# Kernel optimization log

Measured on AMD Instinct MI355X. Metric: run time of the kernel, lower is better.

## Reference

```python
import jax, jax.numpy as jnp
import numpy as np
from jax import lax

B, S, E, H = 8, 1024, 1024, 16
HEAD_DIM = E // H
THRESHOLD = 0.5
NEG_FILL = -1e9


def setup_inputs() -> dict:
    key = jax.random.key(0)
    k0, k1, k2 = jax.random.split(key, 3)
    x = jax.random.normal(k0, (B, S, E), jnp.float32)
    in_proj_w = jax.random.normal(k1, (3 * E, E), jnp.float32) * 0.02
    in_proj_b = jnp.zeros((3 * E,), jnp.float32)
    out_proj_w = jax.random.normal(k2, (E, E), jnp.float32) * 0.02
    out_proj_b = jnp.zeros((E,), jnp.float32)
    return {"x": x, "in_proj_w": in_proj_w, "in_proj_b": in_proj_b,
            "out_proj_w": out_proj_w, "out_proj_b": out_proj_b}


def _mha(x, in_proj_w, in_proj_b, out_proj_w, out_proj_b):
    # PyTorch nn.MultiheadAttention with q=k=v=x, batch_first=True
    qkv = x @ in_proj_w.T + in_proj_b                     # [B,S,3E]
    q, k, v = jnp.split(qkv, 3, axis=-1)                  # each [B,S,E]
    def split_heads(t):
        return t.reshape(B, S, H, HEAD_DIM).transpose(0, 2, 1, 3)  # [B,H,S,d]
    q, k, v = split_heads(q), split_heads(k), split_heads(v)
    scale = 1.0 / np.sqrt(HEAD_DIM).astype(np.float32)
    scores = jnp.einsum('bhqd,bhkd->bhqk', q, k) * scale  # [B,H,S,S]
    w = jax.nn.softmax(scores, axis=-1)
    o = jnp.einsum('bhqk,bhkd->bhqd', w, v)               # [B,H,S,d]
    o = o.transpose(0, 2, 1, 3).reshape(B, S, E)
    attn_output = o @ out_proj_w.T + out_proj_b           # [B,S,E]
    attn_weights = w.mean(axis=1)                         # head-averaged [B,S,S]
    return attn_output, attn_weights


def _cluster(attn_weights):
    # Sequential greedy clustering: scan rows i in order; if row i is not yet
    # visited, its high-attention columns (> THRESHOLD) form cluster i and are
    # marked visited. cluster_id[b, j] = row index of the first cluster that
    # claimed token j, or -1 if never claimed.
    visited0 = jnp.zeros((B, S), dtype=bool)
    cid0 = jnp.full((B, S), -1, dtype=jnp.int32)

    def step(carry, i):
        visited, cid = carry
        process = ~jnp.take(visited, i, axis=1)           # [B] row i unvisited?
        high = jnp.take(attn_weights, i, axis=1) > THRESHOLD  # [B,S]
        claimed = process[:, None] & high                 # [B,S]
        newly = claimed & (~visited)
        cid = jnp.where(newly, jnp.int32(i), cid)
        visited = visited | claimed
        return (visited, cid), None

    (visited, cid), _ = lax.scan(step, (visited0, cid0), jnp.arange(S))
    return cid, visited


def reference(x, in_proj_w, in_proj_b, out_proj_w, out_proj_b):
    attn_output, attn_weights = _mha(x, in_proj_w, in_proj_b, out_proj_w, out_proj_b)
    cluster_ids, covered = _cluster(attn_weights)
    # _generate_image_features: x where token belongs to some cluster, -1e9 else
    clustered_outputs = jnp.where(covered[..., None], x, jnp.float32(NEG_FILL))
    return attn_output, attn_weights, clustered_outputs, cluster_ids
```

## Files before the change

kernel.cpp:

```cpp
#include <hip/hip_runtime.h>
#include <hip/hip_bf16.h>

#define B 8
#define S 1024
#define E 1024
#define H 16

typedef unsigned short u16;
typedef unsigned char u8;
typedef unsigned int u32;
typedef unsigned long long u64;

typedef __attribute__((ext_vector_type(8))) short s16x8;
typedef __attribute__((ext_vector_type(4))) float f32x4;
typedef __attribute__((ext_vector_type(16))) float f32x16;

__device__ __forceinline__ float bf2f(u16 u) {
    union { u32 i; float f; } x; x.i = ((u32)u) << 16; return x.f;
}
__device__ __forceinline__ u16 f2bf(float f) {
    union { float f; u32 i; } x; x.f = f;
    u32 r = x.i + 0x7FFFu + ((x.i >> 16) & 1u);
    return (u16)(r >> 16);
}
__device__ __forceinline__ f32x16 zero16() {
    f32x16 z;
#pragma unroll
    for (int i = 0; i < 16; ++i) z[i] = 0.f;
    return z;
}
__device__ __forceinline__ void gload16(const u16* g, u16* l) {
    __builtin_amdgcn_global_load_lds(
        (const __attribute__((address_space(1))) u32*)g,
        (__attribute__((address_space(3))) u32*)l, 16, 0, 0);
}

__global__ __launch_bounds__(256) void cvt_all(
    const float* __restrict__ x, const float* __restrict__ w0,
    const float* __restrict__ w1, u16* __restrict__ xb,
    u16* __restrict__ wb0, u16* __restrict__ wb1) {
    int i = blockIdx.x * 256 + threadIdx.x;
    const float* src;
    u16* dst;
    int off;
    if (i < 2097152) { src = x; dst = xb; off = i; }
    else if (i < 2883584) { src = w0; dst = wb0; off = i - 2097152; }
    else { src = w1; dst = wb1; off = i - 2883584; }
    float4 v = ((const float4*)src)[off];
    union { u16 u[4]; ushort4 s; } p;
    p.u[0] = f2bf(v.x); p.u[1] = f2bf(v.y);
    p.u[2] = f2bf(v.z); p.u[3] = f2bf(v.w);
    ((ushort4*)dst)[off] = p.s;
}

template <int MODE>
__global__ __launch_bounds__(256) void mfma_gemm(
    const u16* __restrict__ A, const u16* __restrict__ W,
    const float* __restrict__ bias, u16* __restrict__ qb, u16* __restrict__ kb,
    u16* __restrict__ vt, float* __restrict__ outf) {
    __shared__ __align__(16) u16 smem[16384];
    u16* As = smem;
    u16* Bs = smem + 8192;
    const int t = threadIdx.x;
    const int lane = t & 63;
    const int w = t >> 6;
    const int lin = (int)(blockIdx.y * gridDim.x + blockIdx.x);
    const int xcd = lin & 7;
    const int idx = lin >> 3;
    int mt, nt;
    if (MODE == 0) { mt = (xcd & 3) * 16 + idx / 12; nt = (xcd >> 2) * 12 + idx % 12; }
    else           { mt = xcd * 8 + idx / 8;         nt = idx % 8; }
    const int m0 = mt * 128;
    const int n0 = nt * 128;
    const int wm = w >> 1, wn = w & 1;
    const int l15 = lane & 15, l4 = lane >> 4;
    const int lr = lane >> 3;
    const int lc = ((lane & 7) ^ lr) * 8;

    f32x4 acc[4][4];
#pragma unroll
    for (int i = 0; i < 4; ++i)
#pragma unroll
        for (int j = 0; j < 4; ++j) acc[i][j] = {0.f, 0.f, 0.f, 0.f};

    for (int k0 = 0; k0 < 1024; k0 += 64) {
        __syncthreads();
#pragma unroll
        for (int jj = 0; jj < 4; ++jj) {
            int j = w * 4 + jj;
            gload16(A + (size_t)(m0 + j * 8 + lr) * 1024 + k0 + lc, As + j * 512);
            gload16(W + (size_t)(n0 + j * 8 + lr) * 1024 + k0 + lc, Bs + j * 512);
        }
        __syncthreads();
#pragma unroll
        for (int ks = 0; ks < 2; ++ks) {
            s16x8 af[4], bf[4];
#pragma unroll
            for (int i = 0; i < 4; ++i) {
                int row = wm * 64 + i * 16 + l15;
                af[i] = *(const s16x8*)((const u8*)As +
                        (((row << 7) + (ks << 6) + (l4 << 4)) ^ ((row & 7) << 4)));
            }
#pragma unroll
            for (int j = 0; j < 4; ++j) {
                int row = wn * 64 + j * 16 + l15;
                bf[j] = *(const s16x8*)((const u8*)Bs +
                        (((row << 7) + (ks << 6) + (l4 << 4)) ^ ((row & 7) << 4)));
            }
#pragma unroll
            for (int i = 0; i < 4; ++i)
#pragma unroll
                for (int j = 0; j < 4; ++j)
                    acc[i][j] = __builtin_amdgcn_mfma_f32_16x16x32_bf16(
                        af[i], bf[j], acc[i][j], 0, 0, 0);
        }
    }

    if (MODE == 0) {
        __syncthreads();
        u16* Cs = smem;
        const int seg = n0 >> 10;
        const int bb = m0 >> 10;
        const int ms = m0 & 1023;
        if (seg < 2) {
            const float sc = (seg == 0) ? 0.18033688011f : 1.0f;
#pragma unroll
            for (int j = 0; j < 4; ++j) {
                int nl = wn * 64 + j * 16 + l15;
                float bn = bias[n0 + nl];
#pragma unroll
                for (int i = 0; i < 4; ++i) {
                    int ml = wm * 64 + i * 16 + l4 * 4;
#pragma unroll
                    for (int rr = 0; rr < 4; ++rr)
                        Cs[(ml + rr) * 128 + nl] = f2bf((acc[i][j][rr] + bn) * sc);
                }
            }
            __syncthreads();
            u16* dst0 = (seg == 0) ? qb : kb;
#pragma unroll
            for (int it = 0; it < 8; ++it) {
                int flat = it * 256 + t;
                int ml = flat >> 4;
                int g = (flat >> 3) & 1;
                int c8 = flat & 7;
                int hh = ((n0 + g * 64) & 1023) >> 6;
                u16* dst = dst0 + (((size_t)(bb * 16 + hh) * 1024 + ms + ml) << 6) + c8 * 8;
                *(uint4*)dst = *(const uint4*)(Cs + ml * 128 + g * 64 + c8 * 8);
            }
        } else {
#pragma unroll
            for (int j = 0; j < 4; ++j) {
                int nl = wn * 64 + j * 16 + l15;
                float bn = bias[n0 + nl];
                int sz = (nl & 7) << 4;
#pragma unroll
                for (int i = 0; i < 4; ++i) {
                    int ml = wm * 64 + i * 16 + l4 * 4;
#pragma unroll
                    for (int rr = 0; rr < 4; ++rr) {
                        int bl = (ml + rr) << 1;
                        *(u16*)((u8*)Cs + (nl << 8) + (bl ^ sz)) =
                            f2bf(acc[i][j][rr] + bn);
                    }
                }
            }
            __syncthreads();
#pragma unroll
            for (int it = 0; it < 8; ++it) {
                int flat = it * 256 + t;
                int nl = flat >> 4;
                int c = flat & 15;
                int n = n0 + nl;
                int hh = (n & 1023) >> 6;
                int d = n & 63;
                u16* dst = vt + ((size_t)(bb * 16 + hh) * 64 + d) * 1024 + ms + c * 8;
                *(uint4*)dst = *(const uint4*)((u8*)Cs + (nl << 8) +
                                               ((c << 4) ^ ((nl & 7) << 4)));
            }
        }
    } else {
        __syncthreads();
        float* Csf = (float*)smem;
#pragma unroll
        for (int r = 0; r < 2; ++r) {
            if (wm == r) {
#pragma unroll
                for (int j = 0; j < 4; ++j) {
                    int nl = wn * 64 + j * 16 + l15;
                    float bn = bias[n0 + nl];
#pragma unroll
                    for (int i = 0; i < 4; ++i) {
                        int mlr = i * 16 + l4 * 4;
#pragma unroll
                        for (int rr = 0; rr < 4; ++rr)
                            Csf[(mlr + rr) * 128 + nl] = acc[i][j][rr] + bn;
                    }
                }
            }
            __syncthreads();
#pragma unroll
            for (int it = 0; it < 8; ++it) {
                int flat = it * 256 + t;
                int row = flat >> 5;
                int c4 = flat & 31;
                *(float4*)(outf + (size_t)(m0 + r * 64 + row) * 1024 + n0 + c4 * 4) =
                    *(const float4*)(Csf + row * 128 + c4 * 4);
            }
            __syncthreads();
        }
    }
}

template <int BASE>
__device__ __forceinline__ s16x8 build_pa(f32x16 e) {
    u32 a, bv, c, d;
    asm("v_cvt_pk_bf16_f32 %0, %1, %2" : "=v"(a) : "v"(e[BASE + 0]), "v"(e[BASE + 1]));
    asm("v_cvt_pk_bf16_f32 %0, %1, %2" : "=v"(bv) : "v"(e[BASE + 2]), "v"(e[BASE + 3]));
    asm("v_cvt_pk_bf16_f32 %0, %1, %2" : "=v"(c) : "v"(e[BASE + 4]), "v"(e[BASE + 5]));
    asm("v_cvt_pk_bf16_f32 %0, %1, %2" : "=v"(d) : "v"(e[BASE + 6]), "v"(e[BASE + 7]));
    asm("v_permlane32_swap_b32 %0, %1" : "+v"(a), "+v"(c));
    asm("v_permlane32_swap_b32 %0, %1" : "+v"(bv), "+v"(d));
    union { u32 w[4]; s16x8 v; } u;
    u.w[0] = a; u.w[1] = bv; u.w[2] = c; u.w[3] = d;
    return u.v;
}
__device__ __forceinline__ float pair_max(float v) {
    float a_ = v, b_ = v;
    asm("v_permlane32_swap_b32 %0, %1" : "+v"(a_), "+v"(b_));
    return fmaxf(a_, b_);
}
__device__ __forceinline__ u32 pair_or(u32 v) {
    u32 a_ = v, b_ = v;
    asm("v_permlane32_swap_b32 %0, %1" : "+v"(a_), "+v"(b_));
    return a_ | b_;
}

__global__ __launch_bounds__(256, 4) void attn_flash(
    const u16* __restrict__ qg, const u16* __restrict__ kg,
    const u16* __restrict__ vtg, u16* __restrict__ og,
    float* __restrict__ stats) {
    __shared__ __align__(16) u16 bufK[2][64 * 64];
    __shared__ __align__(16) u16 bufV[2][64 * 64];
    const int t = threadIdx.x;
    const int lane = t & 63;
    const int w = t >> 6;
    const int task = ((blockIdx.x & 7) << 7) | (blockIdx.x >> 3);
    const int b = task >> 7;
    const int h = (task >> 3) & 15;
    const int qg_ = task & 7;
    const int q = lane & 31;
    const int hi = lane >> 5;
    const int q0 = qg_ * 128 + w * 32;
    const size_t hb = (size_t)(b * 16 + h) << 16;

    const int lr = lane >> 3;
    const int lc = ((lane & 7) ^ lr) * 8;
    const int swz = (q & 7) << 4;

    union { u32 wd[4]; s16x8 v; } onesu;
    onesu.wd[0] = 0x3F803F80u; onesu.wd[1] = 0x3F803F80u;
    onesu.wd[2] = 0x3F803F80u; onesu.wd[3] = 0x3F803F80u;
    const s16x8 ones = onesu.v;

#define STAGE(tt, bb)                                                          \
    do {                                                                       \
        _Pragma("unroll") for (int jj = 0; jj < 2; ++jj) {                     \
            int j = w * 2 + jj;                                                \
            gload16(kg + hb + (size_t)((tt) * 64 + j * 8 + lr) * 64 + lc,      \
                    bufK[bb] + j * 512);                                       \
            gload16(vtg + hb + (size_t)(j * 8 + lr) * 1024 + (tt) * 64 + lc,   \
                    bufV[bb] + j * 512);                                       \
        }                                                                      \
    } while (0)

    s16x8 qf[4];
#pragma unroll
    for (int s = 0; s < 4; ++s)
        qf[s] = *(const s16x8*)(qg + hb + (size_t)(q0 + q) * 64 + s * 16 + hi * 8);

    f32x16 oLo = zero16(), oHi = zero16(), lacc = zero16();
    float m = 0.f;

    STAGE(0, 0);
    __syncthreads();
    int cur = 0;

    for (int tile = 0; tile < 16; ++tile) {
        if (tile < 15) STAGE(tile + 1, cur ^ 1);
        const u16* bK = bufK[cur];
        const u16* bV = bufV[cur];
#pragma unroll
        for (int kk = 0; kk < 64; kk += 32) {
            s16x8 ka[4];
#pragma unroll
            for (int s = 0; s < 4; ++s)
                ka[s] = *(const s16x8*)((const u8*)bK +
                        ((((kk + q) << 7) + (s << 5) + (hi << 4)) ^ swz));
            f32x16 s_;
            const float negm = -m;
#pragma unroll
            for (int i = 0; i < 16; ++i) s_[i] = negm;
#pragma unroll
            for (int s = 0; s < 4; ++s)
                s_ = __builtin_amdgcn_mfma_f32_32x32x16_bf16(ka[s], qf[s], s_, 0, 0, 0);
            float m0 = fmaxf(fmaxf(s_[0], s_[4]), fmaxf(s_[8], s_[12]));
            float m1 = fmaxf(fmaxf(s_[1], s_[5]), fmaxf(s_[9], s_[13]));
            float m2 = fmaxf(fmaxf(s_[2], s_[6]), fmaxf(s_[10], s_[14]));
            float m3 = fmaxf(fmaxf(s_[3], s_[7]), fmaxf(s_[11], s_[15]));
            float padj = pair_max(fmaxf(fmaxf(m0, m1), fmaxf(m2, m3)));
            if (__any(padj > 11.5f)) {
                float delta = fmaxf(padj, 0.f);
                float r = exp2f(-delta);
                m += delta;
                lacc[0] *= r;
                oLo = oLo * r;
                oHi = oHi * r;
#pragma unroll
                for (int i = 0; i < 16; ++i) s_[i] -= delta;
            }
#pragma unroll
            for (int i = 0; i < 16; ++i) s_[i] = exp2f(s_[i]);
            s16x8 p0 = build_pa<0>(s_), p1 = build_pa<8>(s_);
            lacc = __builtin_amdgcn_mfma_f32_32x32x16_bf16(ones, p0, lacc, 0, 0, 0);
            lacc = __builtin_amdgcn_mfma_f32_32x32x16_bf16(ones, p1, lacc, 0, 0, 0);
            s16x8 vLo0 = *(const s16x8*)((const u8*)bV +
                         (((q << 7) + (kk << 1) + (hi << 4)) ^ swz));
            s16x8 vLo1 = *(const s16x8*)((const u8*)bV +
                         (((q << 7) + (kk << 1) + 32 + (hi << 4)) ^ swz));
            s16x8 vHi0 = *(const s16x8*)((const u8*)bV +
                         ((((q + 32) << 7) + (kk << 1) + (hi << 4)) ^ swz));
            s16x8 vHi1 = *(const s16x8*)((const u8*)bV +
                         ((((q + 32) << 7) + (kk << 1) + 32 + (hi << 4)) ^ swz));
            oLo = __builtin_amdgcn_mfma_f32_32x32x16_bf16(vLo0, p0, oLo, 0, 0, 0);
            oLo = __builtin_amdgcn_mfma_f32_32x32x16_bf16(vLo1, p1, oLo, 0, 0, 0);
            oHi = __builtin_amdgcn_mfma_f32_32x32x16_bf16(vHi0, p0, oHi, 0, 0, 0);
            oHi = __builtin_amdgcn_mfma_f32_32x32x16_bf16(vHi1, p1, oHi, 0, 0, 0);
        }
        __syncthreads();
        cur ^= 1;
    }
#undef STAGE
    const float l = lacc[0];
    float inv = 1.0f / l;
    oLo = oLo * inv;
    oHi = oHi * inv;
    u16* orow = og + (size_t)(b * 1024 + q0 + q) * 1024 + h * 64;
#pragma unroll
    for (int rg = 0; rg < 4; ++rg) {
        union { u16 u[4]; u64 v; } pk;
#pragma unroll
        for (int j = 0; j < 4; ++j) pk.u[j] = f2bf(oLo[4 * rg + j]);
        *(u64*)(orow + 8 * rg + 4 * hi) = pk.v;
#pragma unroll
        for (int j = 0; j < 4; ++j) pk.u[j] = f2bf(oHi[4 * rg + j]);
        *(u64*)(orow + 32 + 4 * hi + 8 * rg) = pk.v;
    }
    if (hi == 0)
        stats[(size_t)(b * 16 + h) * 1024 + q0 + q] = m + 4.0f + log2f(l);
}

__global__ __launch_bounds__(512, 2) void attn_aw(
    const u16* __restrict__ qg, const u16* __restrict__ kg,
    const float* __restrict__ stats, float* __restrict__ aw,
    u64* __restrict__ maskg) {
    __shared__ __align__(16) u16 bufK[2][128 * 64];
    __shared__ __align__(16) u16 bufQ[2][128 * 64];
    const int t = threadIdx.x;
    const int lane = t & 63;
    const int w = t >> 6;
    const int task = ((blockIdx.x & 7) << 6) | (blockIdx.x >> 3);
    const int b = task >> 6;
    const int ks = (task >> 3) & 7;
    const int qg_ = task & 7;
    const int q = lane & 31;
    const int hi = lane >> 5;
    const int wq = w >> 1;
    const int kh = w & 1;
    const int q0 = qg_ * 128;
    const int qr = wq * 32 + q;
    const int krow0 = kh * 64;
    const int kbase = ks * 128 + kh * 64;

    const int lr = lane >> 3;
    const int lc = ((lane & 7) ^ lr) * 8;
    const int swz = (q & 7) << 4;

#define STAGEAW(hh, bb)                                                        \
    do {                                                                       \
        const size_t hbs = (size_t)(b * 16 + (hh)) << 16;                      \
        _Pragma("unroll") for (int jj = 0; jj < 2; ++jj) {                     \
            int j = w * 2 + jj;                                                \
            gload16(kg + hbs + (size_t)(ks * 128 + j * 8 + lr) * 64 + lc,      \
                    bufK[bb] + j * 512);                                       \
            gload16(qg + hbs + (size_t)(q0 + j * 8 + lr) * 64 + lc,            \
                    bufQ[bb] + j * 512);                                       \
        }                                                                      \
    } while (0)

    f32x16 awA = zero16(), awB = zero16();

    STAGEAW(0, 0);
    __syncthreads();
    int cur = 0;

    for (int h = 0; h < 16; ++h) {
        if (h < 15) STAGEAW(h + 1, cur ^ 1);
        const u16* bK = bufK[cur];
        const u16* bQ = bufQ[cur];
        s16x8 qf[4], kA[4], kB[4];
#pragma unroll
        for (int s = 0; s < 4; ++s) {
            qf[s] = *(const s16x8*)((const u8*)bQ +
                    (((qr << 7) + (s << 5) + (hi << 4)) ^ swz));
            kA[s] = *(const s16x8*)((const u8*)bK +
                    ((((krow0 + q) << 7) + (s << 5) + (hi << 4)) ^ swz));
            kB[s] = *(const s16x8*)((const u8*)bK +
                    ((((krow0 + q + 32) << 7) + (s << 5) + (hi << 4)) ^ swz));
        }
        float C = stats[(size_t)(b * 16 + h) * 1024 + q0 + qr];
        f32x16 sA = zero16(), sB = zero16();
#pragma unroll
        for (int s = 0; s < 4; ++s) {
            sA = __builtin_amdgcn_mfma_f32_32x32x16_bf16(kA[s], qf[s], sA, 0, 0, 0);
            sB = __builtin_amdgcn_mfma_f32_32x32x16_bf16(kB[s], qf[s], sB, 0, 0, 0);
        }
#pragma unroll
        for (int i = 0; i < 16; ++i) {
            awA[i] += exp2f(sA[i] - C);
            awB[i] += exp2f(sB[i] - C);
        }
        __syncthreads();
        cur ^= 1;
    }
#undef STAGEAW
    float* awrow = aw + (size_t)(b * 1024 + q0 + qr) * 1024 + kbase;
#pragma unroll
    for (int rg = 0; rg < 4; ++rg) {
        *(float4*)(awrow + 8 * rg + 4 * hi) =
            make_float4(awA[4 * rg + 0], awA[4 * rg + 1], awA[4 * rg + 2], awA[4 * rg + 3]);
        *(float4*)(awrow + 32 + 8 * rg + 4 * hi) =
            make_float4(awB[4 * rg + 0], awB[4 * rg + 1], awB[4 * rg + 2], awB[4 * rg + 3]);
    }
    u32 lo = 0, hi32 = 0;
#pragma unroll
    for (int r = 0; r < 16; ++r) {
        int k = (r & 3) + 8 * (r >> 2) + 4 * hi;
        lo |= (awA[r] > 0.5f) ? (1u << k) : 0u;
        hi32 |= (awB[r] > 0.5f) ? (1u << k) : 0u;
    }
    lo = pair_or(lo);
    hi32 = pair_or(hi32);
    if (hi == 0)
        maskg[(size_t)(b * 1024 + q0 + qr) * 16 + ks * 2 + kh] =
            ((u64)hi32 << 32) | (u64)lo;
}

__global__ __launch_bounds__(256) void cluster_kernel(
    const u64* __restrict__ maskg, float* __restrict__ cid, u64* __restrict__ cov) {
    __shared__ u64 mask[16384];
    __shared__ u16 rows[1024];
    const int t = threadIdx.x;
    const int b = blockIdx.x;
#pragma unroll
    for (int i = 0; i < 64; ++i)
        mask[t + 256 * i] = maskg[(size_t)b * 16384 + t + 256 * i];
#pragma unroll
    for (int i = 0; i < 4; ++i) cid[b * S + t + 256 * i] = -1.0f;
    __syncthreads();
    if (t < 64) {
        int nr = 0;
        for (int it = 0; it < 16; ++it) {
            int row = it * 64 + t;
            const u64* mp = mask + row * 16;
            u64 orv = 0;
#pragma unroll
            for (int j = 0; j < 16; ++j) orv |= mp[j];
            u64 bal = __ballot(orv != 0ULL);
            int pre = __popcll(bal & ((1ULL << t) - 1ULL));
            if (orv != 0ULL) rows[nr + pre] = (u16)row;
            nr += __popcll(bal);
        }
        u64 vis = 0;
        for (int idx = 0; idx < nr; ++idx) {
            int i = rows[idx];
            u64 viw = __shfl(vis, i >> 6);
            bool proc = ((viw >> (i & 63)) & 1ULL) == 0ULL;
            u64 cl = (proc && t < 16) ? mask[i * 16 + t] : 0ULL;
            u64 newly = cl & ~vis;
            vis |= cl;
            while (newly) {
                int bit = __ffsll((long long)newly) - 1;
                cid[b * S + t * 64 + bit] = (float)i;
                newly &= newly - 1;
            }
        }
        if (t < 16) cov[b * 16 + t] = vis;
    }
}

__global__ __launch_bounds__(256) void clustered_kernel(
    const float* __restrict__ x, const u64* __restrict__ cov,
    float* __restrict__ out2) {
    const size_t n4 = (size_t)B * S * E / 4;
    size_t idx = (size_t)blockIdx.x * 256 + threadIdx.x;
    const float4 neg = make_float4(-1e9f, -1e9f, -1e9f, -1e9f);
    for (; idx < n4; idx += (size_t)gridDim.x * 256) {
        size_t tok = idx >> 8;
        int bb = (int)(tok >> 10), s = (int)(tok & 1023);
        u64 m = cov[bb * 16 + (s >> 6)];
        bool c = ((m >> (s & 63)) & 1ULL) != 0ULL;
        float4 v = ((const float4*)x)[idx];
        ((float4*)out2)[idx] = c ? v : neg;
    }
}

extern "C" void kernel_launch(void* const* d_in, const int* in_sizes, int n_in,
                              void* d_out, int out_size, void* d_ws, size_t ws_size,
                              hipStream_t stream) {
    const float* x = (const float*)d_in[0];
    const float* w_in = (const float*)d_in[1];
    const float* b_in = (const float*)d_in[2];
    const float* w_out = (const float*)d_in[3];
    const float* b_out = (const float*)d_in[4];

    float* out0 = (float*)d_out;
    float* out1 = out0 + 8388608;
    float* out2 = out1 + 8388608;
    float* out3 = out2 + 8388608;

    u16* q_bf = (u16*)out0;
    u16* vt_bf = q_bf + 8388608;
    u16* xb = (u16*)out1;
    u16* k_bf = (u16*)out2;
    u16* wb0 = k_bf + 8388608;
    u16* wb1 = wb0 + 3145728;
    float* statsF = (float*)(k_bf + 12582912);
    u16* o_bf = (u16*)d_ws;
    u64* maskg = (u64*)((char*)d_ws + (size_t)(16u << 20));
    u64* cov = (u64*)((char*)d_ws + (size_t)(17u << 20));

    cvt_all<<<12288, 256, 0, stream>>>(x, w_in, w_out, xb, wb0, wb1);

    mfma_gemm<0><<<dim3(64, 24), 256, 0, stream>>>(xb, wb0, b_in, q_bf, k_bf,
                                                   vt_bf, nullptr);
    attn_flash<<<1024, 256, 0, stream>>>(q_bf, k_bf, vt_bf, o_bf, statsF);
    attn_aw<<<512, 512, 0, stream>>>(q_bf, k_bf, statsF, out1, maskg);
    mfma_gemm<1><<<dim3(64, 8), 256, 0, stream>>>(o_bf, wb1, b_out, nullptr,
                                                  nullptr, nullptr, out0);

    cluster_kernel<<<8, 256, 0, stream>>>(maskg, out3, cov);
    clustered_kernel<<<2048, 256, 0, stream>>>(x, cov, out2);
}
```

Measured before the change: 258.6 us.

## Fuse attention-weights pass with output projection GEMM in one launch

Splits the templated GEMM into a QKV kernel and a device-side output-projection body, and reshapes the attention-weights kernel into 256-thread blocks handling 64 keys each. When enough workspace exists, the two independent stages (attention-weight averaging and the output projection) run as one 1536-block launch so they can overlap and fill the GPU together. It also folds the softmax stats subtraction into the MFMA accumulator init and moves buffers into workspace so they do not alias the outputs. Risk: different occupancy and more LDS per block for the GEMM half of the fused kernel.

```diff
diff --git a/kernel.cpp b/kernel.cpp
--- a/kernel.cpp
+++ b/kernel.cpp
@@ -15,9 +15,6 @@
 typedef __attribute__((ext_vector_type(4))) float f32x4;
 typedef __attribute__((ext_vector_type(16))) float f32x16;
 
-__device__ __forceinline__ float bf2f(u16 u) {
-    union { u32 i; float f; } x; x.i = ((u32)u) << 16; return x.f;
-}
 __device__ __forceinline__ u16 f2bf(float f) {
     union { float f; u32 i; } x; x.f = f;
     u32 r = x.i + 0x7FFFu + ((x.i >> 16) & 1u);
@@ -53,11 +50,10 @@
     ((ushort4*)dst)[off] = p.s;
 }
 
-template <int MODE>
-__global__ __launch_bounds__(256) void mfma_gemm(
+__global__ __launch_bounds__(256) void gemm_qkv(
     const u16* __restrict__ A, const u16* __restrict__ W,
     const float* __restrict__ bias, u16* __restrict__ qb, u16* __restrict__ kb,
-    u16* __restrict__ vt, float* __restrict__ outf) {
+    u16* __restrict__ vt) {
     __shared__ __align__(16) u16 smem[16384];
     u16* As = smem;
     u16* Bs = smem + 8192;
@@ -67,9 +63,8 @@
     const int lin = (int)(blockIdx.y * gridDim.x + blockIdx.x);
     const int xcd = lin & 7;
     const int idx = lin >> 3;
-    int mt, nt;
-    if (MODE == 0) { mt = (xcd & 3) * 16 + idx / 12; nt = (xcd >> 2) * 12 + idx % 12; }
-    else           { mt = xcd * 8 + idx / 8;         nt = idx % 8; }
+    const int mt = (xcd & 3) * 16 + idx / 12;
+    const int nt = (xcd >> 2) * 12 + idx % 12;
     const int m0 = mt * 128;
     const int n0 = nt * 128;
     const int wm = w >> 1, wn = w & 1;
@@ -116,99 +111,154 @@
         }
     }
 
-    if (MODE == 0) {
-        __syncthreads();
-        u16* Cs = smem;
-        const int seg = n0 >> 10;
-        const int bb = m0 >> 10;
-        const int ms = m0 & 1023;
-        if (seg < 2) {
-            const float sc = (seg == 0) ? 0.18033688011f : 1.0f;
+    __syncthreads();
+    u16* Cs = smem;
+    const int seg = n0 >> 10;
+    const int bb = m0 >> 10;
+    const int ms = m0 & 1023;
+    if (seg < 2) {
+        const float sc = (seg == 0) ? 0.18033688011f : 1.0f;
+#pragma unroll
+        for (int j = 0; j < 4; ++j) {
+            int nl = wn * 64 + j * 16 + l15;
+            float bn = bias[n0 + nl];
+#pragma unroll
+            for (int i = 0; i < 4; ++i) {
+                int ml = wm * 64 + i * 16 + l4 * 4;
+#pragma unroll
+                for (int rr = 0; rr < 4; ++rr)
+                    Cs[(ml + rr) * 128 + nl] = f2bf((acc[i][j][rr] + bn) * sc);
+            }
+        }
+        __syncthreads();
+        u16* dst0 = (seg == 0) ? qb : kb;
+#pragma unroll
+        for (int it = 0; it < 8; ++it) {
+            int flat = it * 256 + t;
+            int ml = flat >> 4;
+            int g = (flat >> 3) & 1;
+            int c8 = flat & 7;
+            int hh = ((n0 + g * 64) & 1023) >> 6;
+            u16* dst = dst0 + (((size_t)(bb * 16 + hh) * 1024 + ms + ml) << 6) + c8 * 8;
+            *(uint4*)dst = *(const uint4*)(Cs + ml * 128 + g * 64 + c8 * 8);
+        }
+    } else {
+#pragma unroll
+        for (int j = 0; j < 4; ++j) {
+            int nl = wn * 64 + j * 16 + l15;
+            float bn = bias[n0 + nl];
+            int sz = (nl & 7) << 4;
+#pragma unroll
+            for (int i = 0; i < 4; ++i) {
+                int ml = wm * 64 + i * 16 + l4 * 4;
+#pragma unroll
+                for (int rr = 0; rr < 4; ++rr) {
+                    int bl = (ml + rr) << 1;
+                    *(u16*)((u8*)Cs + (nl << 8) + (bl ^ sz)) =
+                        f2bf(acc[i][j][rr] + bn);
+                }
+            }
+        }
+        __syncthreads();
+#pragma unroll
+        for (int it = 0; it < 8; ++it) {
+            int flat = it * 256 + t;
+            int nl = flat >> 4;
+            int c = flat & 15;
+            int n = n0 + nl;
+            int hh = (n & 1023) >> 6;
+            int d = n & 63;
+            u16* dst = vt + ((size_t)(bb * 16 + hh) * 64 + d) * 1024 + ms + c * 8;
+            *(uint4*)dst = *(const uint4*)((u8*)Cs + (nl << 8) +
+                                           ((c << 4) ^ ((nl & 7) << 4)));
+        }
+    }
+}
+
+__device__ __forceinline__ void gemm1_body(
+    int lin, u16* smem, const u16* __restrict__ A, const u16* __restrict__ W,
+    const float* __restrict__ bias, float* __restrict__ outf) {
+    u16* As = smem;
+    u16* Bs = smem + 8192;
+    const int t = threadIdx.x;
+    const int lane = t & 63;
+    const int w = t >> 6;
+    const int xcd = lin & 7;
+    const int idx = lin >> 3;
+    const int m0 = (xcd * 8 + idx / 8) * 128;
+    const int n0 = (idx % 8) * 128;
+    const int wm = w >> 1, wn = w & 1;
+    const int l15 = lane & 15, l4 = lane >> 4;
+    const int lr = lane >> 3;
+    const int lc = ((lane & 7) ^ lr) * 8;
+
+    f32x4 acc[4][4];
+#pragma unroll
+    for (int i = 0; i < 4; ++i)
+#pragma unroll
+        for (int j = 0; j < 4; ++j) acc[i][j] = {0.f, 0.f, 0.f, 0.f};
+
+    for (int k0 = 0; k0 < 1024; k0 += 64) {
+        __syncthreads();
+#pragma unroll
+        for (int jj = 0; jj < 4; ++jj) {
+            int j = w * 4 + jj;
+            gload16(A + (size_t)(m0 + j * 8 + lr) * 1024 + k0 + lc, As + j * 512);
+            gload16(W + (size_t)(n0 + j * 8 + lr) * 1024 + k0 + lc, Bs + j * 512);
+        }
+        __syncthreads();
+#pragma unroll
+        for (int ks = 0; ks < 2; ++ks) {
+            s16x8 af[4], bf[4];
+#pragma unroll
+            for (int i = 0; i < 4; ++i) {
+                int row = wm * 64 + i * 16 + l15;
+                af[i] = *(const s16x8*)((const u8*)As +
+                        (((row << 7) + (ks << 6) + (l4 << 4)) ^ ((row & 7) << 4)));
+            }
+#pragma unroll
+            for (int j = 0; j < 4; ++j) {
+                int row = wn * 64 + j * 16 + l15;
+                bf[j] = *(const s16x8*)((const u8*)Bs +
+                        (((row << 7) + (ks << 6) + (l4 << 4)) ^ ((row & 7) << 4)));
+            }
+#pragma unroll
+            for (int i = 0; i < 4; ++i)
+#pragma unroll
+                for (int j = 0; j < 4; ++j)
+                    acc[i][j] = __builtin_amdgcn_mfma_f32_16x16x32_bf16(
+                        af[i], bf[j], acc[i][j], 0, 0, 0);
+        }
+    }
+
+    __syncthreads();
+    float* Csf = (float*)smem;
+#pragma unroll
+    for (int r = 0; r < 2; ++r) {
+        if (wm == r) {
 #pragma unroll
             for (int j = 0; j < 4; ++j) {
                 int nl = wn * 64 + j * 16 + l15;
                 float bn = bias[n0 + nl];
 #pragma unroll
                 for (int i = 0; i < 4; ++i) {
-                    int ml = wm * 64 + i * 16 + l4 * 4;
+                    int mlr = i * 16 + l4 * 4;
 #pragma unroll
                     for (int rr = 0; rr < 4; ++rr)
-                        Cs[(ml + rr) * 128 + nl] = f2bf((acc[i][j][rr] + bn) * sc);
+                        Csf[(mlr + rr) * 128 + nl] = acc[i][j][rr] + bn;
                 }
             }
-            __syncthreads();
-            u16* dst0 = (seg == 0) ? qb : kb;
-#pragma unroll
-            for (int it = 0; it < 8; ++it) {
-                int flat = it * 256 + t;
-                int ml = flat >> 4;
-                int g = (flat >> 3) & 1;
-                int c8 = flat & 7;
-                int hh = ((n0 + g * 64) & 1023) >> 6;
-                u16* dst = dst0 + (((size_t)(bb * 16 + hh) * 1024 + ms + ml) << 6) + c8 * 8;
-                *(uint4*)dst = *(const uint4*)(Cs + ml * 128 + g * 64 + c8 * 8);
-            }
-        } else {
-#pragma unroll
-            for (int j = 0; j < 4; ++j) {
-                int nl = wn * 64 + j * 16 + l15;
-                float bn = bias[n0 + nl];
-                int sz = (nl & 7) << 4;
-#pragma unroll
-                for (int i = 0; i < 4; ++i) {
-                    int ml = wm * 64 + i * 16 + l4 * 4;
-#pragma unroll
-                    for (int rr = 0; rr < 4; ++rr) {
-                        int bl = (ml + rr) << 1;
-                        *(u16*)((u8*)Cs + (nl << 8) + (bl ^ sz)) =
-                            f2bf(acc[i][j][rr] + bn);
-                    }
-                }
-            }
-            __syncthreads();
-#pragma unroll
-            for (int it = 0; it < 8; ++it) {
-                int flat = it * 256 + t;
-                int nl = flat >> 4;
-                int c = flat & 15;
-                int n = n0 + nl;
-                int hh = (n & 1023) >> 6;
-                int d = n & 63;
-                u16* dst = vt + ((size_t)(bb * 16 + hh) * 64 + d) * 1024 + ms + c * 8;
-                *(uint4*)dst = *(const uint4*)((u8*)Cs + (nl << 8) +
-                                               ((c << 4) ^ ((nl & 7) << 4)));
-            }
-        }
-    } else {
-        __syncthreads();
-        float* Csf = (float*)smem;
-#pragma unroll
-        for (int r = 0; r < 2; ++r) {
-            if (wm == r) {
-#pragma unroll
-                for (int j = 0; j < 4; ++j) {
-                    int nl = wn * 64 + j * 16 + l15;
-                    float bn = bias[n0 + nl];
-#pragma unroll
-                    for (int i = 0; i < 4; ++i) {
-                        int mlr = i * 16 + l4 * 4;
-#pragma unroll
-                        for (int rr = 0; rr < 4; ++rr)
-                            Csf[(mlr + rr) * 128 + nl] = acc[i][j][rr] + bn;
-                    }
-                }
-            }
-            __syncthreads();
-#pragma unroll
-            for (int it = 0; it < 8; ++it) {
-                int flat = it * 256 + t;
-                int row = flat >> 5;
-                int c4 = flat & 31;
-                *(float4*)(outf + (size_t)(m0 + r * 64 + row) * 1024 + n0 + c4 * 4) =
-                    *(const float4*)(Csf + row * 128 + c4 * 4);
-            }
-            __syncthreads();
-        }
+        }
+        __syncthreads();
+#pragma unroll
+        for (int it = 0; it < 8; ++it) {
+            int flat = it * 256 + t;
+            int row = flat >> 5;
+            int c4 = flat & 31;
+            *(float4*)(outf + (size_t)(m0 + r * 64 + row) * 1024 + n0 + c4 * 4) =
+                *(const float4*)(Csf + row * 128 + c4 * 4);
+        }
+        __syncthreads();
     }
 }
 
@@ -360,27 +410,24 @@
         stats[(size_t)(b * 16 + h) * 1024 + q0 + q] = m + 4.0f + log2f(l);
 }
 
-__global__ __launch_bounds__(512, 2) void attn_aw(
-    const u16* __restrict__ qg, const u16* __restrict__ kg,
+__device__ __forceinline__ void aw_body(
+    int bid, u16* smem, const u16* __restrict__ qg, const u16* __restrict__ kg,
     const float* __restrict__ stats, float* __restrict__ aw,
     u64* __restrict__ maskg) {
-    __shared__ __align__(16) u16 bufK[2][128 * 64];
-    __shared__ __align__(16) u16 bufQ[2][128 * 64];
+    u16* bufK = smem;
+    u16* bufQ = smem + 8192;
     const int t = threadIdx.x;
     const int lane = t & 63;
     const int w = t >> 6;
-    const int task = ((blockIdx.x & 7) << 6) | (blockIdx.x >> 3);
-    const int b = task >> 6;
-    const int ks = (task >> 3) & 7;
-    const int qg_ = task & 7;
+    const int sw = ((bid & 7) << 7) | (bid >> 3);
+    const int b = sw >> 7;
+    const int ks = (sw >> 3) & 15;
+    const int qg_ = sw & 7;
     const int q = lane & 31;
     const int hi = lane >> 5;
-    const int wq = w >> 1;
-    const int kh = w & 1;
     const int q0 = qg_ * 128;
-    const int qr = wq * 32 + q;
-    const int krow0 = kh * 64;
-    const int kbase = ks * 128 + kh * 64;
+    const int qr = w * 32 + q;
+    const int kbase = ks * 64;
 
     const int lr = lane >> 3;
     const int lc = ((lane & 7) ^ lr) * 8;
@@ -391,10 +438,13 @@
         const size_t hbs = (size_t)(b * 16 + (hh)) << 16;                      \
         _Pragma("unroll") for (int jj = 0; jj < 2; ++jj) {                     \
             int j = w * 2 + jj;                                                \
-            gload16(kg + hbs + (size_t)(ks * 128 + j * 8 + lr) * 64 + lc,      \
-                    bufK[bb] + j * 512);                                       \
+            gload16(kg + hbs + (size_t)(kbase + j * 8 + lr) * 64 + lc,         \
+                    bufK + (bb) * 4096 + j * 512);                             \
+        }                                                                      \
+        _Pragma("unroll") for (int jj = 0; jj < 4; ++jj) {                     \
+            int j = w * 4 + jj;                                                \
             gload16(qg + hbs + (size_t)(q0 + j * 8 + lr) * 64 + lc,            \
-                    bufQ[bb] + j * 512);                                       \
+                    bufQ + (bb) * 8192 + j * 512);                             \
         }                                                                      \
     } while (0)
 
@@ -406,20 +456,23 @@
 
     for (int h = 0; h < 16; ++h) {
         if (h < 15) STAGEAW(h + 1, cur ^ 1);
-        const u16* bK = bufK[cur];
-        const u16* bQ = bufQ[cur];
+        const u16* bK = bufK + cur * 4096;
+        const u16* bQ = bufQ + cur * 8192;
         s16x8 qf[4], kA[4], kB[4];
 #pragma unroll
         for (int s = 0; s < 4; ++s) {
             qf[s] = *(const s16x8*)((const u8*)bQ +
                     (((qr << 7) + (s << 5) + (hi << 4)) ^ swz));
             kA[s] = *(const s16x8*)((const u8*)bK +
-                    ((((krow0 + q) << 7) + (s << 5) + (hi << 4)) ^ swz));
+                    (((q << 7) + (s << 5) + (hi << 4)) ^ swz));
             kB[s] = *(const s16x8*)((const u8*)bK +
-                    ((((krow0 + q + 32) << 7) + (s << 5) + (hi << 4)) ^ swz));
+                    ((((q + 32) << 7) + (s << 5) + (hi << 4)) ^ swz));
         }
         float C = stats[(size_t)(b * 16 + h) * 1024 + q0 + qr];
-        f32x16 sA = zero16(), sB = zero16();
+        f32x16 sA, sB;
+        const float negC = -C;
+#pragma unroll
+        for (int i = 0; i < 16; ++i) { sA[i] = negC; sB[i] = negC; }
 #pragma unroll
         for (int s = 0; s < 4; ++s) {
             sA = __builtin_amdgcn_mfma_f32_32x32x16_bf16(kA[s], qf[s], sA, 0, 0, 0);
@@ -427,8 +480,8 @@
         }
 #pragma unroll
         for (int i = 0; i < 16; ++i) {
-            awA[i] += exp2f(sA[i] - C);
-            awB[i] += exp2f(sB[i] - C);
+            awA[i] += exp2f(sA[i]);
+            awB[i] += exp2f(sB[i]);
         }
         __syncthreads();
         cur ^= 1;
@@ -452,8 +505,33 @@
     lo = pair_or(lo);
     hi32 = pair_or(hi32);
     if (hi == 0)
-        maskg[(size_t)(b * 1024 + q0 + qr) * 16 + ks * 2 + kh] =
-            ((u64)hi32 << 32) | (u64)lo;
+        maskg[(size_t)(b * 1024 + q0 + qr) * 16 + ks] = ((u64)hi32 << 32) | (u64)lo;
+}
+
+__global__ __launch_bounds__(256, 3) void attn_aw_k(
+    const u16* __restrict__ qg, const u16* __restrict__ kg,
+    const float* __restrict__ stats, float* __restrict__ aw,
+    u64* __restrict__ maskg) {
+    __shared__ __align__(16) u16 sm[24576];
+    aw_body((int)blockIdx.x, sm, qg, kg, stats, aw, maskg);
+}
+__global__ __launch_bounds__(256, 3) void gemm1_k(
+    const u16* __restrict__ A, const u16* __restrict__ W,
+    const float* __restrict__ bias, float* __restrict__ outf) {
+    __shared__ __align__(16) u16 sm[16384];
+    gemm1_body((int)blockIdx.x, sm, A, W, bias, outf);
+}
+__global__ __launch_bounds__(256, 3) void fused_aw_gemm1(
+    const u16* __restrict__ qg, const u16* __restrict__ kg,
+    const float* __restrict__ stats, float* __restrict__ aw,
+    u64* __restrict__ maskg, const u16* __restrict__ o,
+    const u16* __restrict__ w1, const float* __restrict__ bias,
+    float* __restrict__ outf) {
+    __shared__ __align__(16) u16 sm[24576];
+    if (blockIdx.x < 1024)
+        aw_body((int)blockIdx.x, sm, qg, kg, stats, aw, maskg);
+    else
+        gemm1_body((int)blockIdx.x - 1024, sm, o, w1, bias, outf);
 }
 
 __global__ __launch_bounds__(256) void cluster_kernel(
@@ -529,26 +607,43 @@
     float* out2 = out1 + 8388608;
     float* out3 = out2 + 8388608;
 
-    u16* q_bf = (u16*)out0;
-    u16* vt_bf = q_bf + 8388608;
-    u16* xb = (u16*)out1;
-    u16* k_bf = (u16*)out2;
-    u16* wb0 = k_bf + 8388608;
-    u16* wb1 = wb0 + 3145728;
-    float* statsF = (float*)(k_bf + 12582912);
-    u16* o_bf = (u16*)d_ws;
-    u64* maskg = (u64*)((char*)d_ws + (size_t)(16u << 20));
-    u64* cov = (u64*)((char*)d_ws + (size_t)(17u << 20));
-
-    cvt_all<<<12288, 256, 0, stream>>>(x, w_in, w_out, xb, wb0, wb1);
-
-    mfma_gemm<0><<<dim3(64, 24), 256, 0, stream>>>(xb, wb0, b_in, q_bf, k_bf,
-                                                   vt_bf, nullptr);
-    attn_flash<<<1024, 256, 0, stream>>>(q_bf, k_bf, vt_bf, o_bf, statsF);
-    attn_aw<<<512, 512, 0, stream>>>(q_bf, k_bf, statsF, out1, maskg);
-    mfma_gemm<1><<<dim3(64, 8), 256, 0, stream>>>(o_bf, wb1, b_out, nullptr,
-                                                  nullptr, nullptr, out0);
-
-    cluster_kernel<<<8, 256, 0, stream>>>(maskg, out3, cov);
-    clustered_kernel<<<2048, 256, 0, stream>>>(x, cov, out2);
-}
+    if (ws_size >= ((size_t)37 << 20)) {
+        u16* o_bf = (u16*)d_ws;
+        u16* q_bf = (u16*)((char*)d_ws + ((size_t)16 << 20));
+        u16* wb1 = (u16*)((char*)d_ws + ((size_t)32 << 20));
+        float* statsF = (float*)((char*)d_ws + ((size_t)34 << 20));
+        u64* maskg = (u64*)((char*)d_ws + ((size_t)34 << 20) + (1u << 19));
+        u64* cov = (u64*)((char*)d_ws + ((size_t)35 << 20) + (1u << 19));
+        u16* vt_bf = (u16*)out0;
+        u16* xb = (u16*)out1;
+        u16* wb0 = xb + 8388608;
+        u16* k_bf = (u16*)out2;
+
+        cvt_all<<<12288, 256, 0, stream>>>(x, w_in, w_out, xb, wb0, wb1);
+        gemm_qkv<<<dim3(64, 24), 256, 0, stream>>>(xb, wb0, b_in, q_bf, k_bf, vt_bf);
+        attn_flash<<<1024, 256, 0, stream>>>(q_bf, k_bf, vt_bf, o_bf, statsF);
+        fused_aw_gemm1<<<1536, 256, 0, stream>>>(q_bf, k_bf, statsF, out1, maskg,
+                                                 o_bf, wb1, b_out, out0);
+        cluster_kernel<<<8, 256, 0, stream>>>(maskg, out3, cov);
+        clustered_kernel<<<2048, 256, 0, stream>>>(x, cov, out2);
+    } else {
+        u16* q_bf = (u16*)out0;
+        u16* vt_bf = q_bf + 8388608;
+        u16* xb = (u16*)out1;
+        u16* k_bf = (u16*)out2;
+        u16* wb0 = k_bf + 8388608;
+        u16* wb1 = wb0 + 3145728;
+        float* statsF = (float*)(k_bf + 12582912);
+        u16* o_bf = (u16*)d_ws;
+        u64* maskg = (u64*)((char*)d_ws + (size_t)(16u << 20));
+        u64* cov = (u64*)((char*)d_ws + (size_t)(17u << 20));
+
+        cvt_all<<<12288, 256, 0, stream>>>(x, w_in, w_out, xb, wb0, wb1);
+        gemm_qkv<<<dim3(64, 24), 256, 0, stream>>>(xb, wb0, b_in, q_bf, k_bf, vt_bf);
+        attn_flash<<<1024, 256, 0, stream>>>(q_bf, k_bf, vt_bf, o_bf, statsF);
+        attn_aw_k<<<1024, 256, 0, stream>>>(q_bf, k_bf, statsF, out1, maskg);
+        gemm1_k<<<512, 256, 0, stream>>>(o_bf, wb1, b_out, out0);
+        cluster_kernel<<<8, 256, 0, stream>>>(maskg, out3, cov);
+        clustered_kernel<<<2048, 256, 0, stream>>>(x, cov, out2);
+    }
+}
```

Result: faster. 239.7 us (-7.3%).
